# Kernel tuning notes

Measured on AMD Instinct MI355X. Metric: run time of the kernel, lower is better.

## Reference

```python
import math
import jax, jax.numpy as jnp
import numpy as np

MUL = 64
N_ROWS = 131072
L = (0, 1, 2)
# all parity-even triangle-allowed paths (i_in1, i_in2, i_out), connection_mode 'uvu'
PATHS = ((0, 0, 0), (0, 1, 1), (0, 2, 2),
         (1, 0, 1), (1, 1, 0), (1, 1, 1), (1, 1, 2), (1, 2, 1), (1, 2, 2),
         (2, 0, 2), (2, 1, 1), (2, 1, 2), (2, 2, 0), (2, 2, 1), (2, 2, 2))


def _su2_cg(j1, j2, j3, m1, m2, m3):
    # standard SU(2) Clebsch-Gordan coefficient (integer l), matches e3nn
    if m3 != m1 + m2:
        return 0.0
    f = math.factorial
    vmin = max(-j1 + j2 + m3, -j1 + m1, 0)
    vmax = min(j2 + j3 + m1, j3 - j1 + j2, j3 + m3)
    C = math.sqrt((2 * j3 + 1) * f(j3 + j1 - j2) * f(j3 - j1 + j2) * f(j1 + j2 - j3)
                  * f(j3 + m3) * f(j3 - m3)
                  / (f(j1 + j2 + j3 + 1) * f(j1 - m1) * f(j1 + m1) * f(j2 - m2) * f(j2 + m2)))
    S = 0.0
    for v in range(vmin, vmax + 1):
        S += (-1.0) ** (v + j2 + m2) * f(j2 + j3 + m1 - v) * f(j1 - m1 + v) \
             / (f(v) * f(j3 - j1 + j2 - v) * f(j3 + m3 - v) * f(v + j1 - j2 - m3))
    return C * S


def _q(l):
    # change of basis real -> complex spherical harmonics (e3nn convention)
    q = np.zeros((2 * l + 1, 2 * l + 1), dtype=np.complex128)
    for m in range(-l, 0):
        q[l + m, l + abs(m)] = 1 / math.sqrt(2)
        q[l + m, l - abs(m)] = -1j / math.sqrt(2)
    q[l, l] = 1.0
    for m in range(1, l + 1):
        q[l + m, l + abs(m)] = (-1) ** m / math.sqrt(2)
        q[l + m, l - abs(m)] = 1j * (-1) ** m / math.sqrt(2)
    return (-1j) ** l * q


def wigner_3j(l1, l2, l3):
    # real Wigner-3j tensor, Frobenius norm 1, identical to e3nn o3.wigner_3j
    C = np.zeros((2 * l1 + 1, 2 * l2 + 1, 2 * l3 + 1))
    for m1 in range(-l1, l1 + 1):
        for m2 in range(-l2, l2 + 1):
            for m3 in range(-l3, l3 + 1):
                C[l1 + m1, l2 + m2, l3 + m3] = _su2_cg(l1, l2, l3, m1, m2, m3)
    C = C / math.sqrt(2 * l3 + 1)
    W = np.einsum('ij,kl,mn,ikn->jlm', _q(l1), _q(l2), np.conj(_q(l3).T), C.astype(np.complex128))
    assert np.abs(W.imag).max() < 1e-9
    return np.ascontiguousarray(W.real)


# per-path CG tensor with the 'component' normalization coeff sqrt(2*l_out+1) folded in
_W3J = [np.sqrt(2 * L[i3] + 1) * wigner_3j(L[i1], L[i2], L[i3]) for (i1, i2, i3) in PATHS]
# rescale sqrt_k per path: fan_in('uvu') = mul_in2 = 1, summed over paths per out slice
_FAN_IN = {0: 3, 1: 6, 2: 6}
_SQRT_K = np.array([1.0 / math.sqrt(_FAN_IN[i3]) for (_, _, i3) in PATHS], dtype=np.float32)


def setup_inputs() -> dict:
    key = jax.random.key(0)
    k1, k2, k3, k4 = jax.random.split(key, 4)
    x = jax.random.normal(k1, (N_ROWS, 9 * MUL), dtype=jnp.float32)   # 64x0e+64x1e+64x2e
    y = jax.random.normal(k2, (N_ROWS, 9), dtype=jnp.float32)         # 1x0e+1x1e+1x2e
    # internal weights: randn, then scaled in-place by sqrt_k at init (rescale=True)
    weight = jax.random.normal(k3, (len(PATHS), MUL), dtype=jnp.float32) * jnp.asarray(_SQRT_K)[:, None]
    bias = jax.random.normal(k4, (MUL,), dtype=jnp.float32) * 0.02     # bias on the 0e slice
    return {"x": x, "y": y, "weight": weight, "bias": bias}


def reference(x, y, weight, bias):
    N = x.shape[0]
    # split inputs into per-l blocks: [N, mul, 2l+1]
    xs = [x[:, :MUL].reshape(N, MUL, 1),
          x[:, MUL:4 * MUL].reshape(N, MUL, 3),
          x[:, 4 * MUL:9 * MUL].reshape(N, MUL, 5)]
    ys = [y[:, 0:1], y[:, 1:4], y[:, 4:9]]
    outs = [jnp.zeros((N, MUL, d), x.dtype) for d in (1, 3, 5)]
    for p, (i1, i2, i3) in enumerate(PATHS):
        C = jnp.asarray(_W3J[p], dtype=x.dtype)  # [2l1+1, 2l2+1, 2l3+1]
        # 'uvu' path with mul_in2 = 1: out[n,u,k] += w[u] * C[i,j,k] * x[n,u,i] * y[n,j]
        contrib = jnp.einsum('ijk,nui,nj->nuk', C, xs[i1], ys[i2])
        outs[i3] = outs[i3] + contrib * weight[p][None, :, None]
    outs[0] = outs[0] + bias[None, :, None]  # bias only on scalar-even slice
    return jnp.concatenate([o.reshape(N, -1) for o in outs], axis=1)
```

## Files before the change

### kernel.cpp

```cpp
#include <hip/hip_runtime.h>
#include <utility>

namespace w3j {

constexpr int NP = 15;
constexpr int P1[NP] = {0,0,0,1,1,1,1,1,1,2,2,2,2,2,2};
constexpr int P2[NP] = {0,1,2,0,1,1,1,2,2,0,1,1,2,2,2};
constexpr int P3[NP] = {0,1,2,1,0,1,2,1,2,2,1,2,0,1,2};
constexpr int BASE[3] = {0,1,4};

constexpr double cfact(int n){ double r = 1.0; for (int i = 2; i <= n; ++i) r *= i; return r; }
constexpr double csqrt(double x){
  double g = x > 1.0 ? x : 1.0;
  for (int i = 0; i < 64; ++i){ double ng = 0.5*(g + x/g); if (ng == g) break; g = ng; }
  return g;
}
constexpr double neg1pow(int n){ return (n & 1) ? -1.0 : 1.0; }
constexpr int imax3(int a,int b,int c){ int m = a > b ? a : b; return m > c ? m : c; }
constexpr int imin3(int a,int b,int c){ int m = a < b ? a : b; return m < c ? m : c; }

constexpr double su2_cg(int j1,int j2,int j3,int m1,int m2,int m3){
  if (m3 != m1 + m2) return 0.0;
  int vmin = imax3(-j1 + j2 + m3, -j1 + m1, 0);
  int vmax = imin3(j2 + j3 + m1, j3 - j1 + j2, j3 + m3);
  double C = csqrt((2*j3 + 1) * cfact(j3 + j1 - j2) * cfact(j3 - j1 + j2) * cfact(j1 + j2 - j3)
                   * cfact(j3 + m3) * cfact(j3 - m3)
                   / (cfact(j1 + j2 + j3 + 1) * cfact(j1 - m1) * cfact(j1 + m1)
                      * cfact(j2 - m2) * cfact(j2 + m2)));
  double S = 0.0;
  for (int v = vmin; v <= vmax; ++v)
    S += neg1pow(v + j2 + m2) * cfact(j2 + j3 + m1 - v) * cfact(j1 - m1 + v)
         / (cfact(v) * cfact(j3 - j1 + j2 - v) * cfact(j3 + m3 - v) * cfact(v + j1 - j2 - m3));
  return C * S;
}

struct cplx { double re, im; };
constexpr cplx cmul(cplx a, cplx b){ return { a.re*b.re - a.im*b.im, a.re*b.im + a.im*b.re }; }
constexpr cplx cadd(cplx a, cplx b){ return { a.re + b.re, a.im + b.im }; }

struct QM { cplx q[5][5]; };
constexpr QM qmat(int l){
  QM Q{};
  const double is2 = 1.0 / csqrt(2.0);
  for (int m = -l; m < 0; ++m){
    Q.q[l+m][l-m] = cplx{ is2, 0.0 };
    Q.q[l+m][l+m] = cplx{ 0.0, -is2 };
  }
  Q.q[l][l] = cplx{ 1.0, 0.0 };
  for (int m = 1; m <= l; ++m){
    double s = neg1pow(m);
    Q.q[l+m][l+m] = cplx{ s*is2, 0.0 };
    Q.q[l+m][l-m] = cplx{ 0.0, s*is2 };
  }
  cplx f{1.0, 0.0};
  for (int t = 0; t < l; ++t) f = cmul(f, cplx{0.0, -1.0});
  for (int a = 0; a < 2*l+1; ++a) for (int b = 0; b < 2*l+1; ++b) Q.q[a][b] = cmul(Q.q[a][b], f);
  return Q;
}

struct W3 { double w[5][5][5]; };
constexpr W3 wig(int l1,int l2,int l3){
  const int d1 = 2*l1+1, d2 = 2*l2+1, d3 = 2*l3+1;
  double C[5][5][5] = {};
  for (int a = 0; a < d1; ++a) for (int b = 0; b < d2; ++b) for (int c = 0; c < d3; ++c)
    C[a][b][c] = su2_cg(l1, l2, l3, a - l1, b - l2, c - l3);
  const QM q1 = qmat(l1), q2 = qmat(l2), q3 = qmat(l3);
  cplx T1[5][5][5] = {};
  for (int j = 0; j < d1; ++j) for (int k = 0; k < d2; ++k) for (int n = 0; n < d3; ++n){
    cplx s{0,0};
    for (int i = 0; i < d1; ++i) s = cadd(s, cmul(q1.q[i][j], cplx{ C[i][k][n], 0.0 }));
    T1[j][k][n] = s;
  }
  cplx T2[5][5][5] = {};
  for (int j = 0; j < d1; ++j) for (int l = 0; l < d2; ++l) for (int n = 0; n < d3; ++n){
    cplx s{0,0};
    for (int k = 0; k < d2; ++k) s = cadd(s, cmul(q2.q[k][l], T1[j][k][n]));
    T2[j][l][n] = s;
  }
  W3 W{};
  for (int j = 0; j < d1; ++j) for (int l = 0; l < d2; ++l) for (int m = 0; m < d3; ++m){
    cplx s{0,0};
    for (int n = 0; n < d3; ++n)
      s = cadd(s, cmul(cplx{ q3.q[n][m].re, -q3.q[n][m].im }, T2[j][l][n]));
    W.w[j][l][m] = s.re;
  }
  return W;
}

constexpr W3 W_00 = wig(0,0,0);
constexpr W3 W_01 = wig(0,1,1);
constexpr W3 W_02 = wig(0,2,2);
constexpr W3 W_03 = wig(1,0,1);
constexpr W3 W_04 = wig(1,1,0);
constexpr W3 W_05 = wig(1,1,1);
constexpr W3 W_06 = wig(1,1,2);
constexpr W3 W_07 = wig(1,2,1);
constexpr W3 W_08 = wig(1,2,2);
constexpr W3 W_09 = wig(2,0,2);
constexpr W3 W_10 = wig(2,1,1);
constexpr W3 W_11 = wig(2,1,2);
constexpr W3 W_12 = wig(2,2,0);
constexpr W3 W_13 = wig(2,2,1);
constexpr W3 W_14 = wig(2,2,2);

struct Entry { int p, gi, gj, gk; float v; };
struct Table { Entry e[615]; int n; };
constexpr Table build(){
  const W3 WS[NP] = { W_00,W_01,W_02,W_03,W_04,W_05,W_06,W_07,
                      W_08,W_09,W_10,W_11,W_12,W_13,W_14 };
  Table t{};
  for (int p = 0; p < NP; ++p){
    const int l1 = P1[p], l2 = P2[p], l3 = P3[p];
    for (int i = 0; i < 2*l1+1; ++i)
      for (int j = 0; j < 2*l2+1; ++j)
        for (int k = 0; k < 2*l3+1; ++k){
          double v = WS[p].w[i][j][k];
          if (v > 1e-12 || v < -1e-12){
            t.e[t.n] = Entry{ p, BASE[l1] + i, BASE[l2] + j, BASE[l3] + k, (float)v };
            ++t.n;
          }
        }
  }
  return t;
}
constexpr Table TBL = build();
constexpr int NNZ = TBL.n;

}

template<int E>
__device__ __forceinline__ void apply_one(const float (&xx)[9], const float (&yv)[9],
                                          const float (&wp)[w3j::NP], float (&oo)[9]){
  constexpr w3j::Entry en = w3j::TBL.e[E];
  oo[en.gk] = fmaf(wp[en.p] * xx[en.gi] * en.v, yv[en.gj], oo[en.gk]);
}

template<int... Es>
__device__ __forceinline__ void apply_all(std::integer_sequence<int, Es...>,
                                          const float (&xx)[9], const float (&yv)[9],
                                          const float (&wp)[w3j::NP], float (&oo)[9]){
  (apply_one<Es>(xx, yv, wp, oo), ...);
}

__global__ __launch_bounds__(256)
void tp_rescale_kernel(const float* __restrict__ x, const float* __restrict__ y,
                       const float* __restrict__ w, const float* __restrict__ b,
                       float* __restrict__ out, int nrows)
{
  const int t = threadIdx.x;
  const int u = t & 63;
  const long n = (long)blockIdx.x * 4 + (t >> 6);
  if (n >= nrows) return;

  const float* __restrict__ xr = x + n * 576;
  const float* __restrict__ yr = y + n * 9;

  float xx[9], yv[9], wp[w3j::NP], oo[9];

  xx[0] = xr[u];
  #pragma unroll
  for (int i = 0; i < 3; ++i) xx[1 + i] = xr[64 + 3*u + i];
  #pragma unroll
  for (int k = 0; k < 5; ++k) xx[4 + k] = xr[256 + 5*u + k];

  #pragma unroll
  for (int j = 0; j < 9; ++j) yv[j] = yr[j];

  #pragma unroll
  for (int p = 0; p < w3j::NP; ++p) wp[p] = w[p * 64 + u];

  #pragma unroll
  for (int k = 0; k < 9; ++k) oo[k] = 0.0f;

  apply_all(std::make_integer_sequence<int, w3j::NNZ>{}, xx, yv, wp, oo);

  float* __restrict__ orow = out + n * 576;
  orow[u] = oo[0] + b[u];
  #pragma unroll
  for (int i = 0; i < 3; ++i) orow[64 + 3*u + i] = oo[1 + i];
  #pragma unroll
  for (int k = 0; k < 5; ++k) orow[256 + 5*u + k] = oo[4 + k];
}

extern "C" void kernel_launch(void* const* d_in, const int* in_sizes, int n_in,
                              void* d_out, int out_size, void* d_ws, size_t ws_size,
                              hipStream_t stream) {
  const float* x = (const float*)d_in[0];
  const float* y = (const float*)d_in[1];
  const float* w = (const float*)d_in[2];
  const float* b = (const float*)d_in[3];
  float* out = (float*)d_out;

  const int nrows = in_sizes[0] / 576;
  const int blocks = (nrows + 3) / 4;

  hipLaunchKernelGGL(tp_rescale_kernel, dim3(blocks), dim3(256), 0, stream,
                     x, y, w, b, out, nrows);
}
```

Baseline: 120.8 us.

## Stage 16-row tiles through LDS for coalesced float4 loads and stores

Each block now copies 16 rows of x (and y) into shared memory with coalesced float4 loads, computes four rows per wave from LDS, writes the results back into LDS, and stores them to global memory with coalesced float4 writes. This replaces the strided per-thread global accesses (stride 3 and 5 floats), and amortizes the weight and bias loads over four rows. The cost is 36 KB of LDS per block, which limits occupancy, plus the 3- and 5-float stride LDS accesses may cause bank conflicts. The tail check is dropped, so the row count is assumed to be a multiple of 16.

```diff
diff --git a/kernel.cpp b/kernel.cpp
--- a/kernel.cpp
+++ b/kernel.cpp
@@ -142,44 +142,82 @@
   (apply_one<Es>(xx, yv, wp, oo), ...);
 }
 
+constexpr int ROWS = 16;
+constexpr int RF   = 576;
+constexpr int LDSF = ROWS * RF;
+constexpr int V4   = LDSF / 4 / 256;
+
 __global__ __launch_bounds__(256)
 void tp_rescale_kernel(const float* __restrict__ x, const float* __restrict__ y,
                        const float* __restrict__ w, const float* __restrict__ b,
-                       float* __restrict__ out, int nrows)
+                       float* __restrict__ out)
 {
+  __shared__ float lds[LDSF];
+  __shared__ float yl[ROWS * 9];
+
   const int t = threadIdx.x;
+  const long rowbase = (long)blockIdx.x * ROWS;
+
+  {
+    const float4* __restrict__ src = (const float4*)(x + rowbase * RF);
+    float4* dst = (float4*)lds;
+    #pragma unroll
+    for (int i = 0; i < V4; ++i) dst[i * 256 + t] = src[i * 256 + t];
+    if (t < ROWS * 9) yl[t] = y[rowbase * 9 + t];
+  }
+  __syncthreads();
+
   const int u = t & 63;
-  const long n = (long)blockIdx.x * 4 + (t >> 6);
-  if (n >= nrows) return;
-
-  const float* __restrict__ xr = x + n * 576;
-  const float* __restrict__ yr = y + n * 9;
-
-  float xx[9], yv[9], wp[w3j::NP], oo[9];
-
-  xx[0] = xr[u];
-  #pragma unroll
-  for (int i = 0; i < 3; ++i) xx[1 + i] = xr[64 + 3*u + i];
-  #pragma unroll
-  for (int k = 0; k < 5; ++k) xx[4 + k] = xr[256 + 5*u + k];
-
-  #pragma unroll
-  for (int j = 0; j < 9; ++j) yv[j] = yr[j];
-
+  const int wv = t >> 6;
+  float wp[w3j::NP];
   #pragma unroll
   for (int p = 0; p < w3j::NP; ++p) wp[p] = w[p * 64 + u];
-
+  const float bu = b[u];
+
+  float acc[4][9];
   #pragma unroll
-  for (int k = 0; k < 9; ++k) oo[k] = 0.0f;
-
-  apply_all(std::make_integer_sequence<int, w3j::NNZ>{}, xx, yv, wp, oo);
-
-  float* __restrict__ orow = out + n * 576;
-  orow[u] = oo[0] + b[u];
+  for (int r = 0; r < 4; ++r) {
+    const int lr = wv + 4 * r;
+    const float* __restrict__ xr = lds + lr * RF;
+    const float* __restrict__ yr = yl + lr * 9;
+
+    float xx[9], yv[9], oo[9];
+    xx[0] = xr[u];
+    #pragma unroll
+    for (int i = 0; i < 3; ++i) xx[1 + i] = xr[64 + 3 * u + i];
+    #pragma unroll
+    for (int k = 0; k < 5; ++k) xx[4 + k] = xr[256 + 5 * u + k];
+    #pragma unroll
+    for (int j = 0; j < 9; ++j) yv[j] = yr[j];
+    #pragma unroll
+    for (int k = 0; k < 9; ++k) oo[k] = 0.0f;
+
+    apply_all(std::make_integer_sequence<int, w3j::NNZ>{}, xx, yv, wp, oo);
+
+    acc[r][0] = oo[0] + bu;
+    #pragma unroll
+    for (int k = 1; k < 9; ++k) acc[r][k] = oo[k];
+  }
+  __syncthreads();
+
   #pragma unroll
-  for (int i = 0; i < 3; ++i) orow[64 + 3*u + i] = oo[1 + i];
-  #pragma unroll
-  for (int k = 0; k < 5; ++k) orow[256 + 5*u + k] = oo[4 + k];
+  for (int r = 0; r < 4; ++r) {
+    const int lr = wv + 4 * r;
+    float* __restrict__ orow = lds + lr * RF;
+    orow[u] = acc[r][0];
+    #pragma unroll
+    for (int i = 0; i < 3; ++i) orow[64 + 3 * u + i] = acc[r][1 + i];
+    #pragma unroll
+    for (int k = 0; k < 5; ++k) orow[256 + 5 * u + k] = acc[r][4 + k];
+  }
+  __syncthreads();
+
+  {
+    float4* __restrict__ dst = (float4*)(out + rowbase * RF);
+    const float4* src = (const float4*)lds;
+    #pragma unroll
+    for (int i = 0; i < V4; ++i) dst[i * 256 + t] = src[i * 256 + t];
+  }
 }
 
 extern "C" void kernel_launch(void* const* d_in, const int* in_sizes, int n_in,
@@ -192,8 +230,8 @@
   float* out = (float*)d_out;
 
   const int nrows = in_sizes[0] / 576;
-  const int blocks = (nrows + 3) / 4;
+  const int blocks = nrows / ROWS;
 
   hipLaunchKernelGGL(tp_rescale_kernel, dim3(blocks), dim3(256), 0, stream,
-                     x, y, w, b, out, nrows);
-}
+                     x, y, w, b, out);
+}
```

New measurement: 127.0 us. +5.2%, slower.

## Process four rows per wave with vectorized loads and stores

Applied to the files above, without the earlier changes.

Each wavefront now handles four consecutive rows, loading the per-channel weights and bias once and reusing them across rows. The x input and output for the l=1 and l=2 blocks are accessed through 3- and 4-wide vector types. The bounds check is dropped and the grid is sized assuming the row count divides evenly by 16. This trades more registers per thread for fewer redundant weight loads and more memory operations in flight.

```diff
diff --git a/kernel.cpp b/kernel.cpp
--- a/kernel.cpp
+++ b/kernel.cpp
@@ -142,44 +142,62 @@
   (apply_one<Es>(xx, yv, wp, oo), ...);
 }
 
+typedef float f3u __attribute__((ext_vector_type(3), aligned(4)));
+typedef float f4u __attribute__((ext_vector_type(4), aligned(4)));
+
+constexpr int WR = 4;
+constexpr int RF = 576;
+
 __global__ __launch_bounds__(256)
 void tp_rescale_kernel(const float* __restrict__ x, const float* __restrict__ y,
                        const float* __restrict__ w, const float* __restrict__ b,
-                       float* __restrict__ out, int nrows)
+                       float* __restrict__ out)
 {
-  const int t = threadIdx.x;
-  const int u = t & 63;
-  const long n = (long)blockIdx.x * 4 + (t >> 6);
-  if (n >= nrows) return;
-
-  const float* __restrict__ xr = x + n * 576;
-  const float* __restrict__ yr = y + n * 9;
-
-  float xx[9], yv[9], wp[w3j::NP], oo[9];
-
-  xx[0] = xr[u];
-  #pragma unroll
-  for (int i = 0; i < 3; ++i) xx[1 + i] = xr[64 + 3*u + i];
-  #pragma unroll
-  for (int k = 0; k < 5; ++k) xx[4 + k] = xr[256 + 5*u + k];
-
-  #pragma unroll
-  for (int j = 0; j < 9; ++j) yv[j] = yr[j];
-
+  const int t    = threadIdx.x;
+  const int u    = t & 63;
+  const int wv   = __builtin_amdgcn_readfirstlane(t >> 6);
+  const long rowbase = ((long)blockIdx.x * 4 + wv) * WR;
+
+  float xx[WR][9];
+  #pragma unroll
+  for (int r = 0; r < WR; ++r) {
+    const float* xr = x + (rowbase + r) * RF;
+    xx[r][0] = xr[u];
+    f3u a = *(const f3u*)(xr + 64 + 3 * u);
+    f4u c = *(const f4u*)(xr + 256 + 5 * u);
+    float e = xr[256 + 5 * u + 4];
+    xx[r][1] = a[0]; xx[r][2] = a[1]; xx[r][3] = a[2];
+    xx[r][4] = c[0]; xx[r][5] = c[1]; xx[r][6] = c[2]; xx[r][7] = c[3];
+    xx[r][8] = e;
+  }
+
+  float yv[WR][9];
+  #pragma unroll
+  for (int r = 0; r < WR; ++r)
+    #pragma unroll
+    for (int j = 0; j < 9; ++j) yv[r][j] = y[(rowbase + r) * 9 + j];
+
+  float wp[w3j::NP];
   #pragma unroll
   for (int p = 0; p < w3j::NP; ++p) wp[p] = w[p * 64 + u];
-
-  #pragma unroll
-  for (int k = 0; k < 9; ++k) oo[k] = 0.0f;
-
-  apply_all(std::make_integer_sequence<int, w3j::NNZ>{}, xx, yv, wp, oo);
-
-  float* __restrict__ orow = out + n * 576;
-  orow[u] = oo[0] + b[u];
-  #pragma unroll
-  for (int i = 0; i < 3; ++i) orow[64 + 3*u + i] = oo[1 + i];
-  #pragma unroll
-  for (int k = 0; k < 5; ++k) orow[256 + 5*u + k] = oo[4 + k];
+  const float bu = b[u];
+
+  #pragma unroll
+  for (int r = 0; r < WR; ++r) {
+    float oo[9];
+    #pragma unroll
+    for (int k = 0; k < 9; ++k) oo[k] = 0.0f;
+
+    apply_all(std::make_integer_sequence<int, w3j::NNZ>{}, xx[r], yv[r], wp, oo);
+
+    float* orow = out + (rowbase + r) * RF;
+    orow[u] = oo[0] + bu;
+    f3u s1; s1[0] = oo[1]; s1[1] = oo[2]; s1[2] = oo[3];
+    *(f3u*)(orow + 64 + 3 * u) = s1;
+    f4u s2; s2[0] = oo[4]; s2[1] = oo[5]; s2[2] = oo[6]; s2[3] = oo[7];
+    *(f4u*)(orow + 256 + 5 * u) = s2;
+    orow[256 + 5 * u + 4] = oo[8];
+  }
 }
 
 extern "C" void kernel_launch(void* const* d_in, const int* in_sizes, int n_in,
@@ -192,8 +210,8 @@
   float* out = (float*)d_out;
 
   const int nrows = in_sizes[0] / 576;
-  const int blocks = (nrows + 3) / 4;
+  const int blocks = nrows / (4 * WR);
 
   hipLaunchKernelGGL(tp_rescale_kernel, dim3(blocks), dim3(256), 0, stream,
-                     x, y, w, b, out, nrows);
-}
+                     x, y, w, b, out);
+}
```

After: 121.4 us. No clear change (+0.5%).
